# Optimization experiments

Hardware: AMD Instinct MI355X
Metric: run time of the kernel (lower is better)

## Reference

```python
import jax, jax.numpy as jnp
import numpy as np

B, S, D = 1, 2048, 2048
H, KV, HD = 32, 8, 64  # heads, kv heads, head_dim
THETA = 10000.0


def rot(x):
    # torch: cat(-x[..., d/2:], x[..., :d/2])
    f, s = jnp.split(x, 2, axis=-1)
    return jnp.concatenate((-s, f), axis=-1)


def setup_inputs() -> dict:
    key = jax.random.key(0)
    k0, k1, k2, k3, k4 = jax.random.split(key, 5)
    x = jax.random.normal(k0, (B, S, D), jnp.float32)
    Wq = jax.random.normal(k1, (H * HD, D), jnp.float32) * 0.02
    Wk = jax.random.normal(k2, (KV * HD, D), jnp.float32) * 0.02
    Wv = jax.random.normal(k3, (KV * HD, D), jnp.float32) * 0.02
    Wo = jax.random.normal(k4, (D, H * HD), jnp.float32) * 0.02
    inv_freq = 1.0 / (THETA ** (jnp.arange(0, HD, 2, dtype=jnp.float32) / HD))
    return {"x": x, "Wq": Wq, "Wk": Wk, "Wv": Wv, "Wo": Wo, "inv_freq": inv_freq}


def reference(x, Wq, Wk, Wv, Wo, inv_freq):
    bsz, seqlen, _ = x.shape
    q = (x @ Wq.T).reshape(bsz, seqlen, H, HD).transpose(0, 2, 1, 3)   # [B,H,S,hd]
    k = (x @ Wk.T).reshape(bsz, seqlen, KV, HD).transpose(0, 2, 1, 3)  # [B,KV,S,hd]
    v = (x @ Wv.T).reshape(bsz, seqlen, KV, HD).transpose(0, 2, 1, 3)

    # RoPE cos/sin (computed under no_grad in torch)
    pos = jnp.arange(seqlen, dtype=jnp.float32)
    freqs = pos[:, None] * inv_freq[None, :]                # [S, hd/2]
    emb = jnp.concatenate((freqs, freqs), axis=-1)          # [S, hd]
    cos = jnp.cos(emb)[None, None]                          # [1,1,S,hd]
    sin = jnp.sin(emb)[None, None]
    q = q * cos + rot(q) * sin
    k = k * cos + rot(k) * sin

    # GQA: group query heads per kv head instead of repeat_interleaving kv
    G = H // KV
    qg = q.reshape(bsz, KV, G, seqlen, HD)
    scores = jnp.einsum('bkgsd,bktd->bkgst', qg, k) / jnp.sqrt(jnp.float32(HD))
    mask = jnp.triu(jnp.full((seqlen, seqlen), -jnp.inf, jnp.float32), 1)
    attn = jax.nn.softmax(scores + mask, axis=-1)
    out = jnp.einsum('bkgst,bktd->bkgsd', attn, v)          # [B,KV,G,S,hd]
    out = out.reshape(bsz, H, seqlen, HD).transpose(0, 2, 1, 3).reshape(bsz, seqlen, H * HD)
    return out @ Wo.T
```

## Files before the change

### kernel.cpp

```cpp
#include <hip/hip_runtime.h>
#include <hip/hip_bf16.h>
#include <math.h>

#define S_LEN 2048
#define D_MODEL 2048
#define N_H 32
#define N_KV 8
#define HD 64

typedef __attribute__((ext_vector_type(8))) short short8;
typedef __attribute__((ext_vector_type(4))) float floatx4;
typedef unsigned short u16;
typedef unsigned int u32;

#define QSCALE 0.18033688011112042f

#if defined(__has_builtin)
#if __has_builtin(__builtin_amdgcn_exp2f)
#define EXP2(x) __builtin_amdgcn_exp2f(x)
#else
#define EXP2(x) __expf(0.6931471805599453f * (x))
#endif
#else
#define EXP2(x) __expf(0.6931471805599453f * (x))
#endif

__device__ __forceinline__ u16 f2bf(float f) {
    union { float f; u32 u; } v; v.f = f;
    u32 r = v.u + 0x7fffu + ((v.u >> 16) & 1u);
    return (u16)(r >> 16);
}
__device__ __forceinline__ u16 f2bf_fast(float f) {
    union { float f; u32 u; } v; v.f = f;
    return (u16)((v.u + 0x8000u) >> 16);
}

__device__ __forceinline__ void gload16(const void* gp, void* lp) {
    __builtin_amdgcn_global_load_lds(
        (const __attribute__((address_space(1))) unsigned int*)gp,
        (__attribute__((address_space(3))) unsigned int*)lp,
        16, 0, 0);
}

__global__ __launch_bounds__(256) void cast_all(const float* __restrict__ x,
                                                const float* __restrict__ Wq,
                                                const float* __restrict__ Wk,
                                                const float* __restrict__ Wv,
                                                const float* __restrict__ Wo,
                                                u16* __restrict__ xb,
                                                u16* __restrict__ wqkv,
                                                u16* __restrict__ wob) {
    const int i = (blockIdx.x * 256 + threadIdx.x) * 4;
    const int row = i >> 11;
    const int col = i & 2047;
    const float* src;
    u16* dst;
    if (row < 2048)      { src = x  + (size_t)row * 2048 + col;          dst = xb + i; }
    else if (row < 4096) { src = Wq + (size_t)(row - 2048) * 2048 + col; dst = wqkv + (i - 2048 * 2048); }
    else if (row < 4608) { src = Wk + (size_t)(row - 4096) * 2048 + col; dst = wqkv + (i - 2048 * 2048); }
    else if (row < 5120) { src = Wv + (size_t)(row - 4608) * 2048 + col; dst = wqkv + (i - 2048 * 2048); }
    else                 { src = Wo + (size_t)(row - 5120) * 2048 + col; dst = wob + (i - 5120 * 2048); }
    const float4 v = *(const float4*)src;
    ushort4 o;
    o.x = f2bf(v.x); o.y = f2bf(v.y); o.z = f2bf(v.z); o.w = f2bf(v.w);
    *(ushort4*)dst = o;
}

__global__ __launch_bounds__(256) void gemm_qkv(const u16* __restrict__ A,
                                                const u16* __restrict__ B,
                                                u16* __restrict__ Qh,
                                                u16* __restrict__ Kh,
                                                u16* __restrict__ Vt,
                                                const float* __restrict__ inv_freq,
                                                int K) {
    __shared__ u16 As[2][128 * 32];
    __shared__ u16 Bs[2][128 * 32];
    const int tid  = threadIdx.x;
    const int w    = tid >> 6;
    const int lane = tid & 63;
    const int lr   = lane & 15;
    const int quad = lane >> 4;
    const int bm = blockIdx.x * 128, bn = blockIdx.y * 128;
    const int wm = (w & 1) * 64, wn = (w >> 1) * 64;

    const int srow = tid >> 2;
    const int sch  = (tid & 3) * 8;
    const u16* Ag = A + (size_t)(bm + srow) * K + sch;
    const u16* Bg = B + (size_t)(bn + srow) * K + sch;
    const int loff = srow * 32 + sch;
    const size_t gstride = (size_t)64 * K;

    floatx4 acc[4][4];
#pragma unroll
    for (int i = 0; i < 4; ++i)
#pragma unroll
        for (int j = 0; j < 4; ++j) acc[i][j] = floatx4{0.f, 0.f, 0.f, 0.f};

    gload16(Ag, &As[0][loff]);
    gload16(Ag + gstride, &As[0][loff + 64 * 32]);
    gload16(Bg, &Bs[0][loff]);
    gload16(Bg + gstride, &Bs[0][loff + 64 * 32]);
    __syncthreads();

    for (int k0 = 0; k0 < K; k0 += 32) {
        const int cur = (k0 >> 5) & 1;
        if (k0 + 32 < K) {
            gload16(Ag + k0 + 32, &As[cur ^ 1][loff]);
            gload16(Ag + gstride + k0 + 32, &As[cur ^ 1][loff + 64 * 32]);
            gload16(Bg + k0 + 32, &Bs[cur ^ 1][loff]);
            gload16(Bg + gstride + k0 + 32, &Bs[cur ^ 1][loff + 64 * 32]);
        }
        short8 af[4], bf[4];
#pragma unroll
        for (int t = 0; t < 4; ++t) {
            af[t] = *(const short8*)&As[cur][(wm + t * 16 + lr) * 32 + quad * 8];
            bf[t] = *(const short8*)&Bs[cur][(wn + t * 16 + lr) * 32 + quad * 8];
        }
#pragma unroll
        for (int im = 0; im < 4; ++im)
#pragma unroll
            for (int in = 0; in < 4; ++in)
                acc[im][in] = __builtin_amdgcn_mfma_f32_16x16x32_bf16(
                    af[im], bf[in], acc[im][in], 0, 0, 0);
        __syncthreads();
    }

    const int c0 = bn + wn;
    if (bn < 2048) {
        const int h = c0 >> 6;
#pragma unroll
        for (int p = 0; p < 2; ++p) {
            const int d = p * 16 + lr;
            const float fr = inv_freq[d];
#pragma unroll
            for (int im = 0; im < 4; ++im)
#pragma unroll
                for (int r = 0; r < 4; ++r) {
                    const int s = bm + wm + im * 16 + quad * 4 + r;
                    float sn, cs;
                    sincosf((float)s * fr, &sn, &cs);
                    const float xl = acc[im][p][r], xh = acc[im][p + 2][r];
                    u16* qrow = Qh + ((size_t)h * S_LEN + s) * HD;
                    qrow[d]      = f2bf((xl * cs - xh * sn) * QSCALE);
                    qrow[d + 32] = f2bf((xh * cs + xl * sn) * QSCALE);
                }
        }
    } else if (bn < 2560) {
        const int kv = (c0 - 2048) >> 6;
#pragma unroll
        for (int p = 0; p < 2; ++p) {
            const int d = p * 16 + lr;
            const float fr = inv_freq[d];
#pragma unroll
            for (int im = 0; im < 4; ++im)
#pragma unroll
                for (int r = 0; r < 4; ++r) {
                    const int s = bm + wm + im * 16 + quad * 4 + r;
                    float sn, cs;
                    sincosf((float)s * fr, &sn, &cs);
                    const float xl = acc[im][p][r], xh = acc[im][p + 2][r];
                    u16* krow = Kh + ((size_t)kv * S_LEN + s) * HD;
                    krow[d]      = f2bf(xl * cs - xh * sn);
                    krow[d + 32] = f2bf(xh * cs + xl * sn);
                }
        }
    } else {
        const int kv = (c0 - 2560) >> 6;
#pragma unroll
        for (int im = 0; im < 4; ++im)
#pragma unroll
            for (int in = 0; in < 4; ++in) {
                const int dfull = in * 16 + lr;
                const int s0 = bm + wm + im * 16 + quad * 4;
                ushort4 o;
                o.x = f2bf(acc[im][in][0]); o.y = f2bf(acc[im][in][1]);
                o.z = f2bf(acc[im][in][2]); o.w = f2bf(acc[im][in][3]);
                *(ushort4*)&Vt[((size_t)kv * HD + dfull) * S_LEN + s0] = o;
            }
    }
}

__global__ __launch_bounds__(256) void gemm_out(const u16* __restrict__ A,
                                                const u16* __restrict__ B,
                                                float* __restrict__ Cf,
                                                int N, int K) {
    __shared__ u16 As[2][128 * 32];
    __shared__ u16 Bs[2][64 * 32];
    const int tid  = threadIdx.x;
    const int w    = tid >> 6;
    const int lane = tid & 63;
    const int lr   = lane & 15;
    const int quad = lane >> 4;
    const int bm = blockIdx.x * 128, bn = blockIdx.y * 64;
    const int wm = w * 32;

    const int srow = tid >> 2;
    const int sch  = (tid & 3) * 8;
    const u16* Ag0 = A + (size_t)(bm + srow) * K + sch;
    const u16* Ag1 = Ag0 + (size_t)64 * K;
    const u16* Bg  = B + (size_t)(bn + srow) * K + sch;
    const int loff = srow * 32 + sch;

    floatx4 acc[2][4];
#pragma unroll
    for (int i = 0; i < 2; ++i)
#pragma unroll
        for (int j = 0; j < 4; ++j) acc[i][j] = floatx4{0.f, 0.f, 0.f, 0.f};

    gload16(Ag0, &As[0][loff]);
    gload16(Ag1, &As[0][loff + 64 * 32]);
    gload16(Bg, &Bs[0][loff]);
    __syncthreads();

    for (int k0 = 0; k0 < K; k0 += 32) {
        const int cur = (k0 >> 5) & 1;
        if (k0 + 32 < K) {
            gload16(Ag0 + k0 + 32, &As[cur ^ 1][loff]);
            gload16(Ag1 + k0 + 32, &As[cur ^ 1][loff + 64 * 32]);
            gload16(Bg + k0 + 32, &Bs[cur ^ 1][loff]);
        }
        short8 af[2], bf[4];
#pragma unroll
        for (int im = 0; im < 2; ++im)
            af[im] = *(const short8*)&As[cur][(wm + im * 16 + lr) * 32 + quad * 8];
#pragma unroll
        for (int in = 0; in < 4; ++in)
            bf[in] = *(const short8*)&Bs[cur][(in * 16 + lr) * 32 + quad * 8];
#pragma unroll
        for (int im = 0; im < 2; ++im)
#pragma unroll
            for (int in = 0; in < 4; ++in)
                acc[im][in] = __builtin_amdgcn_mfma_f32_16x16x32_bf16(
                    af[im], bf[in], acc[im][in], 0, 0, 0);
        __syncthreads();
    }

#pragma unroll
    for (int im = 0; im < 2; ++im)
#pragma unroll
        for (int in = 0; in < 4; ++in) {
            const int row0 = bm + wm + im * 16 + quad * 4;
            const int col  = bn + in * 16 + lr;
#pragma unroll
            for (int r = 0; r < 4; ++r)
                Cf[(size_t)(row0 + r) * N + col] = acc[im][in][r];
        }
}

__global__ __launch_bounds__(256) void attn_mfma(const u16* __restrict__ Qh,
                                                 const u16* __restrict__ Kh,
                                                 const u16* __restrict__ Vt,
                                                 u16* __restrict__ AO) {
    __shared__ u16 QPs[64 * 64];
    __shared__ u16 Ks[2][64 * 64];
    __shared__ u16 Vs[2][64 * 64];

    const int bid = blockIdx.x;
    const int h   = bid & 31;
    const int qb  = 31 - (bid >> 5);
    const int kv  = h >> 2;
    const int tid  = threadIdx.x;
    const int w    = tid >> 6;
    const int lr   = tid & 15;
    const int quad = (tid >> 4) & 3;
    const int grow = tid >> 3;
    const int gp   = tid & 7;

    const u16* Qg = Qh + ((size_t)h * S_LEN + (size_t)qb * 64) * HD;
    const u16* Kg = Kh + (size_t)kv * S_LEN * HD;
    const u16* Vg = Vt + (size_t)kv * HD * S_LEN;

#pragma unroll
    for (int j = 0; j < 2; ++j) {
        const int r = j * 32 + grow;
        gload16(Qg + (size_t)r * HD + ((gp ^ (r & 7)) * 8), QPs + r * 64 + gp * 8);
        gload16(Kg + (size_t)r * HD + ((gp ^ (r & 7)) * 8), &Ks[0][r * 64 + gp * 8]);
        gload16(Vg + (size_t)r * S_LEN + ((gp ^ (r & 7)) * 8), &Vs[0][r * 64 + gp * 8]);
    }
    __syncthreads();

    const int wq0 = qb * 64 + w * 16;

    short8 qf[2];
#pragma unroll
    for (int kh = 0; kh < 2; ++kh) {
        const int row = w * 16 + lr;
        const int c   = kh * 4 + quad;
        qf[kh] = *(const short8*)&QPs[row * 64 + ((c ^ (row & 7)) * 8)];
    }

    float l_st[4] = {0.f, 0.f, 0.f, 0.f};
    floatx4 oacc[4];
#pragma unroll
    for (int dn = 0; dn < 4; ++dn) oacc[dn] = floatx4{0.f, 0.f, 0.f, 0.f};

    for (int kt = 0; kt <= qb; ++kt) {
        const int buf = kt & 1;
        if (kt < qb) {
            const int nb = buf ^ 1;
#pragma unroll
            for (int j = 0; j < 2; ++j) {
                const int r = j * 32 + grow;
                gload16(Kg + (size_t)((kt + 1) * 64 + r) * HD + ((gp ^ (r & 7)) * 8),
                        &Ks[nb][r * 64 + gp * 8]);
                gload16(Vg + (size_t)r * S_LEN + (kt + 1) * 64 + ((gp ^ (r & 7)) * 8),
                        &Vs[nb][r * 64 + gp * 8]);
            }
        }
        if (64 * kt <= wq0 + 15) {
            floatx4 st[4];
#pragma unroll
            for (int in = 0; in < 4; ++in) st[in] = floatx4{0.f, 0.f, 0.f, 0.f};
#pragma unroll
            for (int in = 0; in < 4; ++in)
#pragma unroll
                for (int kh = 0; kh < 2; ++kh) {
                    const int row = in * 16 + lr;
                    const int c   = kh * 4 + quad;
                    const short8 kf = *(const short8*)
                        &Ks[buf][row * 64 + ((c ^ (row & 7)) * 8)];
                    st[in] = __builtin_amdgcn_mfma_f32_16x16x32_bf16(
                        qf[kh], kf, st[in], 0, 0, 0);
                }

            const bool need_mask = (kt * 64 + 63) > wq0;
#pragma unroll
            for (int r = 0; r < 4; ++r) {
                float ps = 0.f;
#pragma unroll
                for (int in = 0; in < 4; ++in) {
                    float s = st[in][r];
                    if (need_mask) {
                        const int rg = wq0 + quad * 4 + r;
                        const int cg = kt * 64 + in * 16 + lr;
                        if (cg > rg) s = -1e30f;
                    }
                    const float p = EXP2(s);
                    st[in][r] = p;
                    ps += p;
                }
                l_st[r] += ps;
            }

#pragma unroll
            for (int in = 0; in < 4; ++in)
#pragma unroll
                for (int r = 0; r < 4; ++r) {
                    const int prow = w * 16 + quad * 4 + r;
                    const int col  = in * 16 + lr;
                    QPs[prow * 64 + (((col >> 3) ^ (prow & 7)) * 8) + (col & 7)] =
                        f2bf_fast(st[in][r]);
                }

#pragma unroll
            for (int kc = 0; kc < 2; ++kc) {
                const int prow = w * 16 + lr;
                const short8 pf = *(const short8*)
                    &QPs[prow * 64 + (((kc * 4 + quad) ^ (prow & 7)) * 8)];
#pragma unroll
                for (int dn = 0; dn < 4; ++dn) {
                    const int vrow = dn * 16 + lr;
                    const int c    = kc * 4 + quad;
                    const short8 vf = *(const short8*)
                        &Vs[buf][vrow * 64 + ((c ^ (vrow & 7)) * 8)];
                    oacc[dn] = __builtin_amdgcn_mfma_f32_16x16x32_bf16(
                        pf, vf, oacc[dn], 0, 0, 0);
                }
            }
        }
        __syncthreads();
    }

#pragma unroll
    for (int r = 0; r < 4; ++r) {
        float lv = l_st[r];
#pragma unroll
        for (int mk = 1; mk < 16; mk <<= 1)
            lv += __shfl_xor(lv, mk);
        const float inv = 1.f / lv;
        const size_t row = (size_t)(wq0 + quad * 4 + r);
#pragma unroll
        for (int dn = 0; dn < 4; ++dn)
            AO[row * D_MODEL + h * 64 + dn * 16 + lr] =
                f2bf(oacc[dn][r] * inv);
    }
}

extern "C" void kernel_launch(void* const* d_in, const int* in_sizes, int n_in,
                              void* d_out, int out_size, void* d_ws, size_t ws_size,
                              hipStream_t stream) {
    const float* x        = (const float*)d_in[0];
    const float* Wq       = (const float*)d_in[1];
    const float* Wk       = (const float*)d_in[2];
    const float* Wv       = (const float*)d_in[3];
    const float* Wo       = (const float*)d_in[4];
    const float* inv_freq = (const float*)d_in[5];
    float* out = (float*)d_out;

    const size_t ME = 1 << 20;
    u16* xb   = (u16*)d_ws;
    u16* wqkv = xb   + 4 * ME;
    u16* wob  = wqkv + 6 * ME;
    u16* qhb  = wob  + 4 * ME;
    u16* khb  = qhb  + 4 * ME;
    u16* vtb  = khb  + 1 * ME;
    u16* aob  = vtb  + 1 * ME;

    const dim3 b256(256);

    cast_all<<<14336, b256, 0, stream>>>(x, Wq, Wk, Wv, Wo, xb, wqkv, wob);

    gemm_qkv<<<dim3(16, 24), b256, 0, stream>>>(
        xb, wqkv, qhb, khb, vtb, inv_freq, D_MODEL);

    attn_mfma<<<dim3(1024), b256, 0, stream>>>(qhb, khb, vtb, aob);

    gemm_out<<<dim3(16, 32), b256, 0, stream>>>(
        aob, wob, out, D_MODEL, D_MODEL);
}
```

Baseline: 227.6 us.

## Load GEMM MFMA fragments directly from global memory, dropping LDS staging

Both projection GEMMs no longer stage tiles through shared memory. Each wave now loads its MFMA operand fragments straight from global memory into registers, double-buffered in registers across two k-steps, which removes the __syncthreads barriers. Tiles become 64x128 with 2x4 fragments per wave, the grids are reshaped to match, and occupancy hints are added. The aim is to cut LDS traffic and barrier stalls. The cost is that inter-wave reuse now depends on L1/L2, and the 16-byte row-strided global loads are less coalesced.

```diff
diff --git a/kernel.cpp b/kernel.cpp
--- a/kernel.cpp
+++ b/kernel.cpp
@@ -66,63 +66,66 @@
     *(ushort4*)dst = o;
 }
 
-__global__ __launch_bounds__(256) void gemm_qkv(const u16* __restrict__ A,
-                                                const u16* __restrict__ B,
-                                                u16* __restrict__ Qh,
-                                                u16* __restrict__ Kh,
-                                                u16* __restrict__ Vt,
-                                                const float* __restrict__ inv_freq,
-                                                int K) {
-    __shared__ u16 As[2][128 * 32];
-    __shared__ u16 Bs[2][128 * 32];
+__global__ __launch_bounds__(256, 3) void gemm_qkv(const u16* __restrict__ A,
+                                                   const u16* __restrict__ B,
+                                                   u16* __restrict__ Qh,
+                                                   u16* __restrict__ Kh,
+                                                   u16* __restrict__ Vt,
+                                                   const float* __restrict__ inv_freq,
+                                                   int K) {
     const int tid  = threadIdx.x;
     const int w    = tid >> 6;
     const int lane = tid & 63;
     const int lr   = lane & 15;
     const int quad = lane >> 4;
-    const int bm = blockIdx.x * 128, bn = blockIdx.y * 128;
-    const int wm = (w & 1) * 64, wn = (w >> 1) * 64;
-
-    const int srow = tid >> 2;
-    const int sch  = (tid & 3) * 8;
-    const u16* Ag = A + (size_t)(bm + srow) * K + sch;
-    const u16* Bg = B + (size_t)(bn + srow) * K + sch;
-    const int loff = srow * 32 + sch;
-    const size_t gstride = (size_t)64 * K;
-
-    floatx4 acc[4][4];
-#pragma unroll
-    for (int i = 0; i < 4; ++i)
+    const int bm = blockIdx.x * 64, bn = blockIdx.y * 128;
+    const int wm = (w & 1) * 32;
+    const int wn = (w >> 1) * 64;
+
+    const u16* Ap[2];
+    const u16* Bp[4];
+#pragma unroll
+    for (int s = 0; s < 2; ++s)
+        Ap[s] = A + (size_t)(bm + wm + s * 16 + lr) * K + quad * 8;
+#pragma unroll
+    for (int t = 0; t < 4; ++t)
+        Bp[t] = B + (size_t)(bn + wn + t * 16 + lr) * K + quad * 8;
+
+    floatx4 acc[2][4];
+#pragma unroll
+    for (int i = 0; i < 2; ++i)
 #pragma unroll
         for (int j = 0; j < 4; ++j) acc[i][j] = floatx4{0.f, 0.f, 0.f, 0.f};
 
-    gload16(Ag, &As[0][loff]);
-    gload16(Ag + gstride, &As[0][loff + 64 * 32]);
-    gload16(Bg, &Bs[0][loff]);
-    gload16(Bg + gstride, &Bs[0][loff + 64 * 32]);
-    __syncthreads();
-
-    for (int k0 = 0; k0 < K; k0 += 32) {
-        const int cur = (k0 >> 5) & 1;
-        if (k0 + 32 < K) {
-            gload16(Ag + k0 + 32, &As[cur ^ 1][loff]);
-            gload16(Ag + gstride + k0 + 32, &As[cur ^ 1][loff + 64 * 32]);
-            gload16(Bg + k0 + 32, &Bs[cur ^ 1][loff]);
-            gload16(Bg + gstride + k0 + 32, &Bs[cur ^ 1][loff + 64 * 32]);
-        }
-        short8 af[4], bf[4];
-#pragma unroll
-        for (int t = 0; t < 4; ++t) {
-            af[t] = *(const short8*)&As[cur][(wm + t * 16 + lr) * 32 + quad * 8];
-            bf[t] = *(const short8*)&Bs[cur][(wn + t * 16 + lr) * 32 + quad * 8];
-        }
-#pragma unroll
-        for (int im = 0; im < 4; ++im)
+    short8 a0[2], a1[2], b0[4], b1[4];
+#pragma unroll
+    for (int s = 0; s < 2; ++s) a0[s] = *(const short8*)(Ap[s]);
+#pragma unroll
+    for (int t = 0; t < 4; ++t) b0[t] = *(const short8*)(Bp[t]);
+
+    for (int k0 = 0; k0 < K; k0 += 64) {
+#pragma unroll
+        for (int s = 0; s < 2; ++s) a1[s] = *(const short8*)(Ap[s] + k0 + 32);
+#pragma unroll
+        for (int t = 0; t < 4; ++t) b1[t] = *(const short8*)(Bp[t] + k0 + 32);
+#pragma unroll
+        for (int im = 0; im < 2; ++im)
 #pragma unroll
             for (int in = 0; in < 4; ++in)
                 acc[im][in] = __builtin_amdgcn_mfma_f32_16x16x32_bf16(
-                    af[im], bf[in], acc[im][in], 0, 0, 0);
-        __syncthreads();
+                    a0[im], b0[in], acc[im][in], 0, 0, 0);
+        if (k0 + 64 < K) {
+#pragma unroll
+            for (int s = 0; s < 2; ++s) a0[s] = *(const short8*)(Ap[s] + k0 + 64);
+#pragma unroll
+            for (int t = 0; t < 4; ++t) b0[t] = *(const short8*)(Bp[t] + k0 + 64);
+        }
+#pragma unroll
+        for (int im = 0; im < 2; ++im)
+#pragma unroll
+            for (int in = 0; in < 4; ++in)
+                acc[im][in] = __builtin_amdgcn_mfma_f32_16x16x32_bf16(
+                    a1[im], b1[in], acc[im][in], 0, 0, 0);
     }
 
     const int c0 = bn + wn;
@@ -133,7 +136,7 @@
             const int d = p * 16 + lr;
             const float fr = inv_freq[d];
 #pragma unroll
-            for (int im = 0; im < 4; ++im)
+            for (int im = 0; im < 2; ++im)
 #pragma unroll
                 for (int r = 0; r < 4; ++r) {
                     const int s = bm + wm + im * 16 + quad * 4 + r;
@@ -152,7 +155,7 @@
             const int d = p * 16 + lr;
             const float fr = inv_freq[d];
 #pragma unroll
-            for (int im = 0; im < 4; ++im)
+            for (int im = 0; im < 2; ++im)
 #pragma unroll
                 for (int r = 0; r < 4; ++r) {
                     const int s = bm + wm + im * 16 + quad * 4 + r;
@@ -167,7 +170,7 @@
     } else {
         const int kv = (c0 - 2560) >> 6;
 #pragma unroll
-        for (int im = 0; im < 4; ++im)
+        for (int im = 0; im < 2; ++im)
 #pragma unroll
             for (int in = 0; in < 4; ++in) {
                 const int dfull = in * 16 + lr;
@@ -180,26 +183,27 @@
     }
 }
 
-__global__ __launch_bounds__(256) void gemm_out(const u16* __restrict__ A,
-                                                const u16* __restrict__ B,
-                                                float* __restrict__ Cf,
-                                                int N, int K) {
-    __shared__ u16 As[2][128 * 32];
-    __shared__ u16 Bs[2][64 * 32];
+__global__ __launch_bounds__(256, 2) void gemm_out(const u16* __restrict__ A,
+                                                   const u16* __restrict__ B,
+                                                   float* __restrict__ Cf,
+                                                   int N, int K) {
     const int tid  = threadIdx.x;
     const int w    = tid >> 6;
     const int lane = tid & 63;
     const int lr   = lane & 15;
     const int quad = lane >> 4;
-    const int bm = blockIdx.x * 128, bn = blockIdx.y * 64;
-    const int wm = w * 32;
-
-    const int srow = tid >> 2;
-    const int sch  = (tid & 3) * 8;
-    const u16* Ag0 = A + (size_t)(bm + srow) * K + sch;
-    const u16* Ag1 = Ag0 + (size_t)64 * K;
-    const u16* Bg  = B + (size_t)(bn + srow) * K + sch;
-    const int loff = srow * 32 + sch;
+    const int bm = blockIdx.x * 64, bn = blockIdx.y * 128;
+    const int wm = (w & 1) * 32;
+    const int wn = (w >> 1) * 64;
+
+    const u16* Ap[2];
+    const u16* Bp[4];
+#pragma unroll
+    for (int s = 0; s < 2; ++s)
+        Ap[s] = A + (size_t)(bm + wm + s * 16 + lr) * K + quad * 8;
+#pragma unroll
+    for (int t = 0; t < 4; ++t)
+        Bp[t] = B + (size_t)(bn + wn + t * 16 + lr) * K + quad * 8;
 
     floatx4 acc[2][4];
 #pragma unroll
@@ -207,32 +211,35 @@
 #pragma unroll
         for (int j = 0; j < 4; ++j) acc[i][j] = floatx4{0.f, 0.f, 0.f, 0.f};
 
-    gload16(Ag0, &As[0][loff]);
-    gload16(Ag1, &As[0][loff + 64 * 32]);
-    gload16(Bg, &Bs[0][loff]);
-    __syncthreads();
-
-    for (int k0 = 0; k0 < K; k0 += 32) {
-        const int cur = (k0 >> 5) & 1;
-        if (k0 + 32 < K) {
-            gload16(Ag0 + k0 + 32, &As[cur ^ 1][loff]);
-            gload16(Ag1 + k0 + 32, &As[cur ^ 1][loff + 64 * 32]);
-            gload16(Bg + k0 + 32, &Bs[cur ^ 1][loff]);
-        }
-        short8 af[2], bf[4];
+    short8 a0[2], a1[2], b0[4], b1[4];
+#pragma unroll
+    for (int s = 0; s < 2; ++s) a0[s] = *(const short8*)(Ap[s]);
+#pragma unroll
+    for (int t = 0; t < 4; ++t) b0[t] = *(const short8*)(Bp[t]);
+
+    for (int k0 = 0; k0 < K; k0 += 64) {
+#pragma unroll
+        for (int s = 0; s < 2; ++s) a1[s] = *(const short8*)(Ap[s] + k0 + 32);
+#pragma unroll
+        for (int t = 0; t < 4; ++t) b1[t] = *(const short8*)(Bp[t] + k0 + 32);
 #pragma unroll
         for (int im = 0; im < 2; ++im)
-            af[im] = *(const short8*)&As[cur][(wm + im * 16 + lr) * 32 + quad * 8];
-#pragma unroll
-        for (int in = 0; in < 4; ++in)
-            bf[in] = *(const short8*)&Bs[cur][(in * 16 + lr) * 32 + quad * 8];
+#pragma unroll
+            for (int in = 0; in < 4; ++in)
+                acc[im][in] = __builtin_amdgcn_mfma_f32_16x16x32_bf16(
+                    a0[im], b0[in], acc[im][in], 0, 0, 0);
+        if (k0 + 64 < K) {
+#pragma unroll
+            for (int s = 0; s < 2; ++s) a0[s] = *(const short8*)(Ap[s] + k0 + 64);
+#pragma unroll
+            for (int t = 0; t < 4; ++t) b0[t] = *(const short8*)(Bp[t] + k0 + 64);
+        }
 #pragma unroll
         for (int im = 0; im < 2; ++im)
 #pragma unroll
             for (int in = 0; in < 4; ++in)
                 acc[im][in] = __builtin_amdgcn_mfma_f32_16x16x32_bf16(
-                    af[im], bf[in], acc[im][in], 0, 0, 0);
-        __syncthreads();
+                    a1[im], b1[in], acc[im][in], 0, 0, 0);
     }
 
 #pragma unroll
@@ -240,7 +247,7 @@
 #pragma unroll
         for (int in = 0; in < 4; ++in) {
             const int row0 = bm + wm + im * 16 + quad * 4;
-            const int col  = bn + in * 16 + lr;
+            const int col  = bn + wn + in * 16 + lr;
 #pragma unroll
             for (int r = 0; r < 4; ++r)
                 Cf[(size_t)(row0 + r) * N + col] = acc[im][in][r];
@@ -410,11 +417,11 @@
 
     cast_all<<<14336, b256, 0, stream>>>(x, Wq, Wk, Wv, Wo, xb, wqkv, wob);
 
-    gemm_qkv<<<dim3(16, 24), b256, 0, stream>>>(
+    gemm_qkv<<<dim3(32, 24), b256, 0, stream>>>(
         xb, wqkv, qhb, khb, vtb, inv_freq, D_MODEL);
 
     attn_mfma<<<dim3(1024), b256, 0, stream>>>(qhb, khb, vtb, aob);
 
-    gemm_out<<<dim3(16, 32), b256, 0, stream>>>(
+    gemm_out<<<dim3(32, 16), b256, 0, stream>>>(
         aob, wob, out, D_MODEL, D_MODEL);
 }
```

New measurement: 360.2 us. 58.2% more time.
